# Kernel tuning notes

Hardware: AMD Instinct MI355X
Metric: run time of the kernel (lower is better)

The kernel has to match this reference:

```python
import jax, jax.numpy as jnp
import numpy as np

D_MODEL = 128
NHEAD = 8
HEAD_DIM = D_MODEL // NHEAD  # 16
NUM_LAYERS = 7
NUM_LABELS = 2
N_NODES = 10000
N_EDGES = 160000
NEG_SLOPE = 0.2  # GATv2Conv default negative_slope


def setup_inputs() -> dict:
    key = jax.random.key(0)
    ks = jax.random.split(key, 10)
    s = 1.0 / np.sqrt(D_MODEL)
    inp = {}
    inp["x"] = jax.random.normal(ks[0], (N_NODES, D_MODEL), dtype=jnp.float32)
    inp["edge_index"] = jax.random.randint(ks[1], (2, N_EDGES), 0, N_NODES, dtype=jnp.int64)
    inp["nchunks"] = 8  # uniform extra chunk size -> chunk = NUM_LABELS + 8 = 10
    # per-layer GATv2 params, stacked on a leading layer axis
    inp["Wl"] = jax.random.normal(ks[2], (NUM_LAYERS, D_MODEL, NHEAD * HEAD_DIM), dtype=jnp.float32) * s
    inp["bl"] = jnp.zeros((NUM_LAYERS, NHEAD * HEAD_DIM), dtype=jnp.float32)
    inp["Wr"] = jax.random.normal(ks[3], (NUM_LAYERS, D_MODEL, NHEAD * HEAD_DIM), dtype=jnp.float32) * s
    inp["br"] = jnp.zeros((NUM_LAYERS, NHEAD * HEAD_DIM), dtype=jnp.float32)
    inp["att"] = jax.random.normal(ks[4], (NUM_LAYERS, NHEAD, HEAD_DIM), dtype=jnp.float32) * s
    inp["bias"] = jnp.zeros((NUM_LAYERS, NHEAD * HEAD_DIM), dtype=jnp.float32)
    # split head: Linear(d_model, 1)
    inp["w_head"] = jax.random.normal(ks[5], (D_MODEL, 1), dtype=jnp.float32) * s
    inp["b_head"] = jnp.zeros((1,), dtype=jnp.float32)
    return inp


def _gatv2_layer(x, src, dst, Wl, bl, Wr, br, att, bias):
    # GATv2: e_ij = a^T LeakyReLU(W_l x_j + W_r x_i); alpha = segment-softmax over dst; out_i = sum alpha * W_l x_j
    N = x.shape[0]
    xl = (x @ Wl + bl).reshape(N, NHEAD, HEAD_DIM)
    xr = (x @ Wr + br).reshape(N, NHEAD, HEAD_DIM)
    z = jax.nn.leaky_relu(xl[src] + xr[dst], NEG_SLOPE)          # [E, H, D]
    e = jnp.einsum('ehd,hd->eh', z, att)                          # [E, H]
    emax = jax.ops.segment_max(e, dst, num_segments=N)            # [N, H]
    ex = jnp.exp(e - emax[dst])
    denom = jax.ops.segment_sum(ex, dst, num_segments=N)          # [N, H]
    alpha = ex / (denom[dst] + 1e-16)                             # [E, H]
    out = jax.ops.segment_sum(alpha[..., None] * xl[src], dst, num_segments=N)  # [N, H, D]
    return out.reshape(N, NHEAD * HEAD_DIM) + bias


def reference(x, edge_index, nchunks, Wl, bl, Wr, br, att, bias, w_head, b_head):
    N = x.shape[0]
    loop = jnp.arange(N, dtype=edge_index.dtype)  # GATv2Conv add_self_loops=True
    src = jnp.concatenate([edge_index[0], loop])
    dst = jnp.concatenate([edge_index[1], loop])
    for i in range(NUM_LAYERS):
        x = _gatv2_layer(x, src, dst, Wl[i], bl[i], Wr[i], br[i], att[i], bias[i])
    # uniform split of size (NUM_LABELS + nchunks); keep first NUM_LABELS rows of each chunk
    chunk = NUM_LABELS + int(nchunks)
    xs = x.reshape(-1, chunk, D_MODEL)[:, :NUM_LABELS]            # [n_chunks, num_labels, d]
    out = (xs @ w_head + b_head)[..., 0]                          # [n_chunks, num_labels]
    return out
```

## Files before the change

### kernel.cpp

```cpp
#include <hip/hip_runtime.h>
#include <math.h>

#define NT 256

typedef __attribute__((ext_vector_type(8))) short bf16x8;
typedef __attribute__((ext_vector_type(4))) float f32x4;


__device__ inline int detect_is64(const int* __restrict__ ei) {
    int is64 = 1;
#pragma unroll
    for (int k = 1; k < 16; k += 2) is64 &= (ei[k] == 0);
    return is64;
}

__device__ inline void split1(float f, short& hi, short& lo) {
    unsigned u = __float_as_uint(f);
    hi = (short)(u >> 16);
    float fl = f - __uint_as_float(u & 0xffff0000u);
    lo = (short)(__float_as_uint(fl) >> 16);
}

__device__ inline void cvt8(const float4& a, const float4& b, bf16x8& hi, bf16x8& lo) {
    float f[8] = {a.x, a.y, a.z, a.w, b.x, b.y, b.z, b.w};
#pragma unroll
    for (int j = 0; j < 8; j++) {
        unsigned u = __float_as_uint(f[j]);
        hi[j] = (short)(u >> 16);
        float fl = f[j] - __uint_as_float(u & 0xffff0000u);
        lo[j] = (short)(__float_as_uint(fl) >> 16);
    }
}


__global__ __launch_bounds__(256) void count_prep(const int* __restrict__ ei, int E, int N,
                                                  int* __restrict__ deg,
                                                  const float* __restrict__ Wl,
                                                  const float* __restrict__ Wr,
                                                  short* __restrict__ Whi,
                                                  short* __restrict__ Wlo) {
    __shared__ float Wt[128][17];
    int t = threadIdx.x;
    if (blockIdx.x < 112) {
        int l = blockIdx.x >> 4;
        int tile = blockIdx.x & 15;
        int c0 = tile * 16;
        const float* Wsrc = (c0 < 128) ? Wl + (size_t)l * 16384 : Wr + (size_t)l * 16384;
        int cbase = (c0 < 128) ? c0 : c0 - 128;
#pragma unroll
        for (int it = 0; it < 8; it++) {
            int idx = it * 256 + t;
            int k = idx >> 4, c = idx & 15;
            Wt[k][c] = Wsrc[(size_t)k * 128 + cbase + c];
        }
        __syncthreads();
        int kt = t >> 6, lane = t & 63, q = (lane >> 4), cl = lane & 15;
        bf16x8 hi, lo;
#pragma unroll
        for (int j = 0; j < 8; j++) {
            short h, lw;
            split1(Wt[kt * 32 + q * 8 + j][cl], h, lw);
            hi[j] = h; lo[j] = lw;
        }
        size_t off = ((((size_t)l * 16 + tile) * 4 + kt) * 64 + lane) * 8;
        *(bf16x8*)(Whi + off) = hi;
        *(bf16x8*)(Wlo + off) = lo;
    } else {
        int e = (blockIdx.x - 112) * 256 + t;
        if (e >= E) return;
        int is64 = detect_is64(ei);
        long long pos = (long long)E + e;
        int d = ei[is64 ? 2 * pos : pos];
        if ((unsigned)d < (unsigned)N) atomicAdd(&deg[d], 1);
    }
}

__global__ __launch_bounds__(256) void scan_kernel(const int* __restrict__ deg,
                                                   int* __restrict__ off,
                                                   int* __restrict__ cur, int N) {
    __shared__ int wsum[4];
    int t = threadIdx.x;
    int per = (N + 255) >> 8;
    int b0 = t * per;
    int s = 0;
    for (int k = 0; k < per; k++) {
        int idx = b0 + k;
        if (idx < N) s += deg[idx];
    }
    int lane = t & 63, w = t >> 6;
    int v = s;
#pragma unroll
    for (int o = 1; o < 64; o <<= 1) {
        int u = __shfl_up(v, o, 64);
        if (lane >= o) v += u;
    }
    if (lane == 63) wsum[w] = v;
    __syncthreads();
    if (t == 0) {
        int r = 0;
#pragma unroll
        for (int j = 0; j < 4; j++) { int xx = wsum[j]; wsum[j] = r; r += xx; }
        off[N] = r;
    }
    __syncthreads();
    int run = v - s + wsum[w];
    for (int k = 0; k < per; k++) {
        int idx = b0 + k;
        if (idx < N) {
            off[idx] = run;
            cur[idx] = run;
            run += deg[idx];
        }
    }
}

__global__ void fill_kernel(const int* __restrict__ ei, int E, int N,
                            int* __restrict__ cur, int* __restrict__ esrc) {
    int e = blockIdx.x * blockDim.x + threadIdx.x;
    if (e >= E) return;
    int is64 = detect_is64(ei);
    long long spos = e, dpos = (long long)E + e;
    int s = ei[is64 ? 2 * spos : spos];
    int d = ei[is64 ? 2 * dpos : dpos];
    if ((unsigned)d >= (unsigned)N || (unsigned)s >= (unsigned)N) return;
    int p = atomicAdd(&cur[d], 1);
    esrc[p] = s;
}


__global__ __launch_bounds__(512)
__attribute__((amdgpu_waves_per_eu(2, 2)))
void gemm_xlxr(const float* __restrict__ x,
               const short* __restrict__ WhiL,
               const short* __restrict__ WloL,
               const float* __restrict__ blv,
               const float* __restrict__ brv,
               float* __restrict__ xl,
               float* __restrict__ xr,
               int N, int ntiles) {
    int t = threadIdx.x;
    int w = t >> 6, lane = t & 63, q = lane >> 4, cl = lane & 15;

    bf16x8 Bh[2][4], Bl[2][4];
    float biasv[2];
    float* outp[2];
    int colc[2];
#pragma unroll
    for (int nt = 0; nt < 2; nt++) {
        int tile = w * 2 + nt;
        int col = tile * 16 + cl;
        if (col < 128) { biasv[nt] = blv[col]; outp[nt] = xl; colc[nt] = col; }
        else           { biasv[nt] = brv[col - 128]; outp[nt] = xr; colc[nt] = col - 128; }
#pragma unroll
        for (int kt = 0; kt < 4; kt++) {
            size_t off = (((size_t)tile * 4 + kt) * 64 + lane) * 8;
            Bh[nt][kt] = *(const bf16x8*)(WhiL + off);
            Bl[nt][kt] = *(const bf16x8*)(WloL + off);
        }
    }

    int rt = blockIdx.x;
    if (rt >= ntiles) return;
    float4 cur[8], nxt[8];
    {
        int row = rt * 16 + cl;
        if (row >= N) row = N - 1;
        const float* ap = x + (size_t)row * 128 + q * 8;
#pragma unroll
        for (int kt = 0; kt < 4; kt++) {
            cur[2 * kt]     = *(const float4*)(ap + kt * 32);
            cur[2 * kt + 1] = *(const float4*)(ap + kt * 32 + 4);
        }
    }

    for (; rt < ntiles; rt += gridDim.x) {
        int rn = rt + gridDim.x;
        if (rn < ntiles) {
            int row = rn * 16 + cl;
            if (row >= N) row = N - 1;
            const float* ap = x + (size_t)row * 128 + q * 8;
#pragma unroll
            for (int kt = 0; kt < 4; kt++) {
                nxt[2 * kt]     = *(const float4*)(ap + kt * 32);
                nxt[2 * kt + 1] = *(const float4*)(ap + kt * 32 + 4);
            }
        }

        bf16x8 Ah[4], Al[4];
#pragma unroll
        for (int kt = 0; kt < 4; kt++) cvt8(cur[2 * kt], cur[2 * kt + 1], Ah[kt], Al[kt]);

        f32x4 acc0 = {0.f, 0.f, 0.f, 0.f}, acc1 = {0.f, 0.f, 0.f, 0.f};
#pragma unroll
        for (int kt = 0; kt < 4; kt++) {
            acc0 = __builtin_amdgcn_mfma_f32_16x16x32_bf16(Ah[kt], Bh[0][kt], acc0, 0, 0, 0);
            acc1 = __builtin_amdgcn_mfma_f32_16x16x32_bf16(Ah[kt], Bh[1][kt], acc1, 0, 0, 0);
            acc0 = __builtin_amdgcn_mfma_f32_16x16x32_bf16(Al[kt], Bh[0][kt], acc0, 0, 0, 0);
            acc1 = __builtin_amdgcn_mfma_f32_16x16x32_bf16(Al[kt], Bh[1][kt], acc1, 0, 0, 0);
            acc0 = __builtin_amdgcn_mfma_f32_16x16x32_bf16(Ah[kt], Bl[0][kt], acc0, 0, 0, 0);
            acc1 = __builtin_amdgcn_mfma_f32_16x16x32_bf16(Ah[kt], Bl[1][kt], acc1, 0, 0, 0);
        }

#pragma unroll
        for (int nt = 0; nt < 2; nt++) {
            f32x4 a = nt ? acc1 : acc0;
#pragma unroll
            for (int r = 0; r < 4; r++) {
                int row = rt * 16 + q * 4 + r;
                if (row < N) outp[nt][(size_t)row * 128 + colc[nt]] = a[r] + biasv[nt];
            }
        }
#pragma unroll
        for (int j = 0; j < 8; j++) cur[j] = nxt[j];
    }
}


__global__ __launch_bounds__(256) void gat_agg(const float4* __restrict__ xl4,
                                               const float4* __restrict__ xr4,
                                               const int* __restrict__ off,
                                               const int* __restrict__ esrc,
                                               const float4* __restrict__ att4,
                                               const float4* __restrict__ bias4,
                                               float4* __restrict__ out4, int N) {
    int lane = threadIdx.x & 63;
    int sub = lane >> 4;
    int cl = lane & 15;
    int i = blockIdx.x * 4 + (threadIdx.x >> 6);
    if (i >= N) return;

    float4 xrA = xr4[(size_t)i * 32 + 2 * cl];
    float4 xrB = xr4[(size_t)i * 32 + 2 * cl + 1];
    float4 atA = att4[2 * cl];
    float4 atB = att4[2 * cl + 1];
    int start = off[i];
    int total = off[i + 1] - start + 1;
    int groups = (total + 3) >> 2;

    int k0 = sub;
    int s0 = (k0 < total) ? ((k0 == 0) ? i : esrc[start + k0 - 1]) : i;
    int k1 = 4 + sub;
    int s1 = (k1 < total) ? esrc[start + k1 - 1] : i;
    float4 v0A = xl4[(size_t)s0 * 32 + 2 * cl];
    float4 v0B = xl4[(size_t)s0 * 32 + 2 * cl + 1];
    int k2 = 8 + sub;
    int s2 = (k2 < total) ? esrc[start + k2 - 1] : i;
    float4 v1A = xl4[(size_t)s1 * 32 + 2 * cl];
    float4 v1B = xl4[(size_t)s1 * 32 + 2 * cl + 1];

    float s = 0.f;
    float4 aA = make_float4(0.f, 0.f, 0.f, 0.f);
    float4 aB = make_float4(0.f, 0.f, 0.f, 0.f);

    for (int g = 0; g < groups; g++) {
        int k3 = 4 * (g + 3) + sub;
        int s3 = (k3 < total) ? esrc[start + k3 - 1] : i;
        float4 v2A = xl4[(size_t)s2 * 32 + 2 * cl];
        float4 v2B = xl4[(size_t)s2 * 32 + 2 * cl + 1];

        int kc = 4 * g + sub;
        int valid = kc < total;
        float z0 = v0A.x + xrA.x, z1 = v0A.y + xrA.y, z2 = v0A.z + xrA.z, z3 = v0A.w + xrA.w;
        float z4 = v0B.x + xrB.x, z5 = v0B.y + xrB.y, z6 = v0B.z + xrB.z, z7 = v0B.w + xrB.w;
        z0 = (z0 > 0.f) ? z0 : 0.2f * z0;
        z1 = (z1 > 0.f) ? z1 : 0.2f * z1;
        z2 = (z2 > 0.f) ? z2 : 0.2f * z2;
        z3 = (z3 > 0.f) ? z3 : 0.2f * z3;
        z4 = (z4 > 0.f) ? z4 : 0.2f * z4;
        z5 = (z5 > 0.f) ? z5 : 0.2f * z5;
        z6 = (z6 > 0.f) ? z6 : 0.2f * z6;
        z7 = (z7 > 0.f) ? z7 : 0.2f * z7;
        float p = z0 * atA.x + z1 * atA.y + z2 * atA.z + z3 * atA.w
                + z4 * atB.x + z5 * atB.y + z6 * atB.z + z7 * atB.w;
        p += __shfl_xor(p, 1, 64);
        p = fminf(fmaxf(p, -80.f), 80.f);
        float wgt = valid ? __expf(p) : 0.f;
        s += wgt;
        aA.x += wgt * v0A.x; aA.y += wgt * v0A.y; aA.z += wgt * v0A.z; aA.w += wgt * v0A.w;
        aB.x += wgt * v0B.x; aB.y += wgt * v0B.y; aB.z += wgt * v0B.z; aB.w += wgt * v0B.w;

        v0A = v1A; v0B = v1B;
        v1A = v2A; v1B = v2B;
        s2 = s3;
    }

#pragma unroll
    for (int o = 16; o <= 32; o <<= 1) {
        s += __shfl_xor(s, o, 64);
        aA.x += __shfl_xor(aA.x, o, 64); aA.y += __shfl_xor(aA.y, o, 64);
        aA.z += __shfl_xor(aA.z, o, 64); aA.w += __shfl_xor(aA.w, o, 64);
        aB.x += __shfl_xor(aB.x, o, 64); aB.y += __shfl_xor(aB.y, o, 64);
        aB.z += __shfl_xor(aB.z, o, 64); aB.w += __shfl_xor(aB.w, o, 64);
    }
    if (sub == 0) {
        float inv = 1.f / (s + 1e-16f);
        float4 bA = bias4[2 * cl], bB = bias4[2 * cl + 1];
        float4 oA, oB;
        oA.x = aA.x * inv + bA.x; oA.y = aA.y * inv + bA.y;
        oA.z = aA.z * inv + bA.z; oA.w = aA.w * inv + bA.w;
        oB.x = aB.x * inv + bB.x; oB.y = aB.y * inv + bB.y;
        oB.z = aB.z * inv + bB.z; oB.w = aB.w * inv + bB.w;
        out4[(size_t)i * 32 + 2 * cl] = oA;
        out4[(size_t)i * 32 + 2 * cl + 1] = oB;
    }
}


__global__ __launch_bounds__(128) void head_kernel(const float* __restrict__ x,
                                                   const float* __restrict__ w,
                                                   const float* __restrict__ bh,
                                                   const int* __restrict__ nch,
                                                   float* __restrict__ out) {
    __shared__ float r[2];
    int b = blockIdx.x, t = threadIdx.x;
    int chunk = 2 + nch[0];
    int row = (b >> 1) * chunk + (b & 1);
    float p = x[(size_t)row * 128 + t] * w[t];
#pragma unroll
    for (int o = 32; o >= 1; o >>= 1) p += __shfl_xor(p, o, 64);
    if ((t & 63) == 0) r[t >> 6] = p;
    __syncthreads();
    if (t == 0) out[b] = r[0] + r[1] + bh[0];
}


extern "C" void kernel_launch(void* const* d_in, const int* in_sizes, int n_in,
                              void* d_out, int out_size, void* d_ws, size_t ws_size,
                              hipStream_t stream) {
    const float* x0 = (const float*)d_in[0];
    const int* ei = (const int*)d_in[1];
    const int* nchunks = (const int*)d_in[2];
    const float* Wl = (const float*)d_in[3];
    const float* bl = (const float*)d_in[4];
    const float* Wr = (const float*)d_in[5];
    const float* br = (const float*)d_in[6];
    const float* att = (const float*)d_in[7];
    const float* bias = (const float*)d_in[8];
    const float* wh = (const float*)d_in[9];
    const float* bh = (const float*)d_in[10];

    const int D = 128;
    int N = in_sizes[0] / D;
    int E = in_sizes[1] / 2;
    int ntiles = (N + 15) / 16;

    size_t fN = (size_t)N * D;
    const size_t WFRAG = 16 * 4 * 64 * 8;
    float* xl = (float*)d_ws;
    float* xr = xl + fN;
    float* xA = xr + fN;
    float* xB = xA + fN;
    short* Whi = (short*)(xB + fN);
    short* Wlo = Whi + 7 * WFRAG;
    int* deg = (int*)(Wlo + 7 * WFRAG);
    int* off = deg + N;
    int* cur = off + N + 1;
    int* esrc = cur + N;

    hipMemsetAsync(deg, 0, (size_t)N * sizeof(int), stream);
    count_prep<<<112 + (E + NT - 1) / NT, NT, 0, stream>>>(ei, E, N, deg, Wl, Wr, Whi, Wlo);
    scan_kernel<<<1, 256, 0, stream>>>(deg, off, cur, N);
    fill_kernel<<<(E + NT - 1) / NT, NT, 0, stream>>>(ei, E, N, cur, esrc);

    int aggblocks = (N + 3) / 4;
    const float* xc = x0;
    float* xn = xA;
    for (int l = 0; l < 7; l++) {
        gemm_xlxr<<<256, 512, 0, stream>>>(xc, Whi + (size_t)l * WFRAG, Wlo + (size_t)l * WFRAG,
                                           bl + (size_t)l * D, br + (size_t)l * D,
                                           xl, xr, N, ntiles);
        gat_agg<<<aggblocks, 256, 0, stream>>>((const float4*)xl, (const float4*)xr, off, esrc,
                                               (const float4*)(att + (size_t)l * D),
                                               (const float4*)(bias + (size_t)l * D),
                                               (float4*)xn, N);
        xc = xn;
        xn = (xn == xA) ? xB : xA;
    }
    head_kernel<<<out_size, 128, 0, stream>>>(xc, wh, bh, nchunks, (float*)d_out);
}
```

Before: 319.3 us.

## Remap gat_agg lanes to 8 edges per wave and fuse head into last layer

Changes the aggregation kernel so each wave handles 8 edges at once, with 8 lanes per edge and each lane covering one full head of 16 floats. This removes the cross-lane shuffle in the attention dot product but drops the software prefetch pipeline of neighbour rows. The final linear head is fused into the last layer's aggregation, which removes a separate kernel launch. The gemm launch attributes are also changed from waves_per_eu(2,2) to launch_bounds(512,1). The gather now loads 64 bytes per lane and needs more accumulator registers, which may lower occupancy.

```diff
diff --git a/kernel.cpp b/kernel.cpp
--- a/kernel.cpp
+++ b/kernel.cpp
@@ -128,19 +128,16 @@
 }
 
 
-__global__ __launch_bounds__(512)
-__attribute__((amdgpu_waves_per_eu(2, 2)))
-void gemm_xlxr(const float* __restrict__ x,
-               const short* __restrict__ WhiL,
-               const short* __restrict__ WloL,
-               const float* __restrict__ blv,
-               const float* __restrict__ brv,
-               float* __restrict__ xl,
-               float* __restrict__ xr,
-               int N, int ntiles) {
+__global__ __launch_bounds__(512, 1) void gemm_xlxr(const float* __restrict__ x,
+                                                    const short* __restrict__ WhiL,
+                                                    const short* __restrict__ WloL,
+                                                    const float* __restrict__ blv,
+                                                    const float* __restrict__ brv,
+                                                    float* __restrict__ xl,
+                                                    float* __restrict__ xr,
+                                                    int N, int ntiles) {
     int t = threadIdx.x;
     int w = t >> 6, lane = t & 63, q = lane >> 4, cl = lane & 15;
-
     bf16x8 Bh[2][4], Bl[2][4];
     float biasv[2];
     float* outp[2];
@@ -158,7 +155,6 @@
             Bl[nt][kt] = *(const bf16x8*)(WloL + off);
         }
     }
-
     int rt = blockIdx.x;
     if (rt >= ntiles) return;
     float4 cur[8], nxt[8];
@@ -172,7 +168,6 @@
             cur[2 * kt + 1] = *(const float4*)(ap + kt * 32 + 4);
         }
     }
-
     for (; rt < ntiles; rt += gridDim.x) {
         int rn = rt + gridDim.x;
         if (rn < ntiles) {
@@ -185,11 +180,9 @@
                 nxt[2 * kt + 1] = *(const float4*)(ap + kt * 32 + 4);
             }
         }
-
         bf16x8 Ah[4], Al[4];
 #pragma unroll
         for (int kt = 0; kt < 4; kt++) cvt8(cur[2 * kt], cur[2 * kt + 1], Ah[kt], Al[kt]);
-
         f32x4 acc0 = {0.f, 0.f, 0.f, 0.f}, acc1 = {0.f, 0.f, 0.f, 0.f};
 #pragma unroll
         for (int kt = 0; kt < 4; kt++) {
@@ -200,7 +193,6 @@
             acc0 = __builtin_amdgcn_mfma_f32_16x16x32_bf16(Ah[kt], Bl[0][kt], acc0, 0, 0, 0);
             acc1 = __builtin_amdgcn_mfma_f32_16x16x32_bf16(Ah[kt], Bl[1][kt], acc1, 0, 0, 0);
         }
-
 #pragma unroll
         for (int nt = 0; nt < 2; nt++) {
             f32x4 a = nt ? acc1 : acc0;
@@ -222,105 +214,103 @@
                                                const int* __restrict__ esrc,
                                                const float4* __restrict__ att4,
                                                const float4* __restrict__ bias4,
-                                               float4* __restrict__ out4, int N) {
+                                               float4* __restrict__ out4, int N,
+                                               int do_head,
+                                               const float* __restrict__ wh,
+                                               const float* __restrict__ bh,
+                                               const int* __restrict__ nch,
+                                               float* __restrict__ head_out) {
     int lane = threadIdx.x & 63;
-    int sub = lane >> 4;
-    int cl = lane & 15;
+    int sub = lane >> 3;
+    int hd = lane & 7;
     int i = blockIdx.x * 4 + (threadIdx.x >> 6);
     if (i >= N) return;
 
-    float4 xrA = xr4[(size_t)i * 32 + 2 * cl];
-    float4 xrB = xr4[(size_t)i * 32 + 2 * cl + 1];
-    float4 atA = att4[2 * cl];
-    float4 atB = att4[2 * cl + 1];
+    int base = hd * 4;
+    float4 xr0 = xr4[(size_t)i * 32 + base];
+    float4 xr1 = xr4[(size_t)i * 32 + base + 1];
+    float4 xr2 = xr4[(size_t)i * 32 + base + 2];
+    float4 xr3 = xr4[(size_t)i * 32 + base + 3];
+    float4 at0 = att4[base], at1 = att4[base + 1], at2 = att4[base + 2], at3 = att4[base + 3];
+
     int start = off[i];
     int total = off[i + 1] - start + 1;
-    int groups = (total + 3) >> 2;
-
-    int k0 = sub;
-    int s0 = (k0 < total) ? ((k0 == 0) ? i : esrc[start + k0 - 1]) : i;
-    int k1 = 4 + sub;
-    int s1 = (k1 < total) ? esrc[start + k1 - 1] : i;
-    float4 v0A = xl4[(size_t)s0 * 32 + 2 * cl];
-    float4 v0B = xl4[(size_t)s0 * 32 + 2 * cl + 1];
-    int k2 = 8 + sub;
-    int s2 = (k2 < total) ? esrc[start + k2 - 1] : i;
-    float4 v1A = xl4[(size_t)s1 * 32 + 2 * cl];
-    float4 v1B = xl4[(size_t)s1 * 32 + 2 * cl + 1];
+    int groups = (total + 7) >> 3;
 
     float s = 0.f;
-    float4 aA = make_float4(0.f, 0.f, 0.f, 0.f);
-    float4 aB = make_float4(0.f, 0.f, 0.f, 0.f);
+    float4 a0 = make_float4(0.f, 0.f, 0.f, 0.f);
+    float4 a1 = a0, a2 = a0, a3 = a0;
 
     for (int g = 0; g < groups; g++) {
-        int k3 = 4 * (g + 3) + sub;
-        int s3 = (k3 < total) ? esrc[start + k3 - 1] : i;
-        float4 v2A = xl4[(size_t)s2 * 32 + 2 * cl];
-        float4 v2B = xl4[(size_t)s2 * 32 + 2 * cl + 1];
-
-        int kc = 4 * g + sub;
-        int valid = kc < total;
-        float z0 = v0A.x + xrA.x, z1 = v0A.y + xrA.y, z2 = v0A.z + xrA.z, z3 = v0A.w + xrA.w;
-        float z4 = v0B.x + xrB.x, z5 = v0B.y + xrB.y, z6 = v0B.z + xrB.z, z7 = v0B.w + xrB.w;
-        z0 = (z0 > 0.f) ? z0 : 0.2f * z0;
-        z1 = (z1 > 0.f) ? z1 : 0.2f * z1;
-        z2 = (z2 > 0.f) ? z2 : 0.2f * z2;
-        z3 = (z3 > 0.f) ? z3 : 0.2f * z3;
-        z4 = (z4 > 0.f) ? z4 : 0.2f * z4;
-        z5 = (z5 > 0.f) ? z5 : 0.2f * z5;
-        z6 = (z6 > 0.f) ? z6 : 0.2f * z6;
-        z7 = (z7 > 0.f) ? z7 : 0.2f * z7;
-        float p = z0 * atA.x + z1 * atA.y + z2 * atA.z + z3 * atA.w
-                + z4 * atB.x + z5 * atB.y + z6 * atB.z + z7 * atB.w;
-        p += __shfl_xor(p, 1, 64);
+        int k = 8 * g + sub;
+        int valid = k < total;
+        int src = valid ? ((k == 0) ? i : esrc[start + k - 1]) : i;
+        const float4* vp = xl4 + (size_t)src * 32 + base;
+        float4 v0 = vp[0], v1 = vp[1], v2 = vp[2], v3 = vp[3];
+
+        float p = 0.f;
+#define LR(zv, xrv, atv)                                            \
+        {                                                            \
+            float z;                                                 \
+            z = zv.x + xrv.x; z = (z > 0.f) ? z : 0.2f * z; p += z * atv.x; \
+            z = zv.y + xrv.y; z = (z > 0.f) ? z : 0.2f * z; p += z * atv.y; \
+            z = zv.z + xrv.z; z = (z > 0.f) ? z : 0.2f * z; p += z * atv.z; \
+            z = zv.w + xrv.w; z = (z > 0.f) ? z : 0.2f * z; p += z * atv.w; \
+        }
+        LR(v0, xr0, at0) LR(v1, xr1, at1) LR(v2, xr2, at2) LR(v3, xr3, at3)
+#undef LR
         p = fminf(fmaxf(p, -80.f), 80.f);
         float wgt = valid ? __expf(p) : 0.f;
         s += wgt;
-        aA.x += wgt * v0A.x; aA.y += wgt * v0A.y; aA.z += wgt * v0A.z; aA.w += wgt * v0A.w;
-        aB.x += wgt * v0B.x; aB.y += wgt * v0B.y; aB.z += wgt * v0B.z; aB.w += wgt * v0B.w;
-
-        v0A = v1A; v0B = v1B;
-        v1A = v2A; v1B = v2B;
-        s2 = s3;
-    }
-
-#pragma unroll
-    for (int o = 16; o <= 32; o <<= 1) {
+        a0.x += wgt * v0.x; a0.y += wgt * v0.y; a0.z += wgt * v0.z; a0.w += wgt * v0.w;
+        a1.x += wgt * v1.x; a1.y += wgt * v1.y; a1.z += wgt * v1.z; a1.w += wgt * v1.w;
+        a2.x += wgt * v2.x; a2.y += wgt * v2.y; a2.z += wgt * v2.z; a2.w += wgt * v2.w;
+        a3.x += wgt * v3.x; a3.y += wgt * v3.y; a3.z += wgt * v3.z; a3.w += wgt * v3.w;
+    }
+
+#pragma unroll
+    for (int o = 8; o <= 32; o <<= 1) {
         s += __shfl_xor(s, o, 64);
-        aA.x += __shfl_xor(aA.x, o, 64); aA.y += __shfl_xor(aA.y, o, 64);
-        aA.z += __shfl_xor(aA.z, o, 64); aA.w += __shfl_xor(aA.w, o, 64);
-        aB.x += __shfl_xor(aB.x, o, 64); aB.y += __shfl_xor(aB.y, o, 64);
-        aB.z += __shfl_xor(aB.z, o, 64); aB.w += __shfl_xor(aB.w, o, 64);
-    }
-    if (sub == 0) {
-        float inv = 1.f / (s + 1e-16f);
-        float4 bA = bias4[2 * cl], bB = bias4[2 * cl + 1];
-        float4 oA, oB;
-        oA.x = aA.x * inv + bA.x; oA.y = aA.y * inv + bA.y;
-        oA.z = aA.z * inv + bA.z; oA.w = aA.w * inv + bA.w;
-        oB.x = aB.x * inv + bB.x; oB.y = aB.y * inv + bB.y;
-        oB.z = aB.z * inv + bB.z; oB.w = aB.w * inv + bB.w;
-        out4[(size_t)i * 32 + 2 * cl] = oA;
-        out4[(size_t)i * 32 + 2 * cl + 1] = oB;
-    }
-}
-
-
-__global__ __launch_bounds__(128) void head_kernel(const float* __restrict__ x,
-                                                   const float* __restrict__ w,
-                                                   const float* __restrict__ bh,
-                                                   const int* __restrict__ nch,
-                                                   float* __restrict__ out) {
-    __shared__ float r[2];
-    int b = blockIdx.x, t = threadIdx.x;
-    int chunk = 2 + nch[0];
-    int row = (b >> 1) * chunk + (b & 1);
-    float p = x[(size_t)row * 128 + t] * w[t];
-#pragma unroll
-    for (int o = 32; o >= 1; o >>= 1) p += __shfl_xor(p, o, 64);
-    if ((t & 63) == 0) r[t >> 6] = p;
-    __syncthreads();
-    if (t == 0) out[b] = r[0] + r[1] + bh[0];
+        a0.x += __shfl_xor(a0.x, o, 64); a0.y += __shfl_xor(a0.y, o, 64);
+        a0.z += __shfl_xor(a0.z, o, 64); a0.w += __shfl_xor(a0.w, o, 64);
+        a1.x += __shfl_xor(a1.x, o, 64); a1.y += __shfl_xor(a1.y, o, 64);
+        a1.z += __shfl_xor(a1.z, o, 64); a1.w += __shfl_xor(a1.w, o, 64);
+        a2.x += __shfl_xor(a2.x, o, 64); a2.y += __shfl_xor(a2.y, o, 64);
+        a2.z += __shfl_xor(a2.z, o, 64); a2.w += __shfl_xor(a2.w, o, 64);
+        a3.x += __shfl_xor(a3.x, o, 64); a3.y += __shfl_xor(a3.y, o, 64);
+        a3.z += __shfl_xor(a3.z, o, 64); a3.w += __shfl_xor(a3.w, o, 64);
+    }
+
+    float inv = 1.f / (s + 1e-16f);
+    float4 b0 = bias4[base], b1 = bias4[base + 1], b2 = bias4[base + 2], b3 = bias4[base + 3];
+    float4 o0, o1, o2, o3;
+    o0.x = a0.x * inv + b0.x; o0.y = a0.y * inv + b0.y; o0.z = a0.z * inv + b0.z; o0.w = a0.w * inv + b0.w;
+    o1.x = a1.x * inv + b1.x; o1.y = a1.y * inv + b1.y; o1.z = a1.z * inv + b1.z; o1.w = a1.w * inv + b1.w;
+    o2.x = a2.x * inv + b2.x; o2.y = a2.y * inv + b2.y; o2.z = a2.z * inv + b2.z; o2.w = a2.w * inv + b2.w;
+    o3.x = a3.x * inv + b3.x; o3.y = a3.y * inv + b3.y; o3.z = a3.z * inv + b3.z; o3.w = a3.w * inv + b3.w;
+
+    if (!do_head) {
+        if (sub == 0) {
+            float4* op = out4 + (size_t)i * 32 + base;
+            op[0] = o0; op[1] = o1; op[2] = o2; op[3] = o3;
+        }
+    } else {
+        int chunk = 2 + nch[0];
+        int ci = i / chunk;
+        int m = i - ci * chunk;
+        if (m < 2) {
+            const float4* wv = (const float4*)wh + base;
+            float4 w0 = wv[0], w1 = wv[1], w2 = wv[2], w3 = wv[3];
+            float p = o0.x * w0.x + o0.y * w0.y + o0.z * w0.z + o0.w * w0.w
+                    + o1.x * w1.x + o1.y * w1.y + o1.z * w1.z + o1.w * w1.w
+                    + o2.x * w2.x + o2.y * w2.y + o2.z * w2.z + o2.w * w2.w
+                    + o3.x * w3.x + o3.y * w3.y + o3.z * w3.z + o3.w * w3.w;
+            p += __shfl_xor(p, 1, 64);
+            p += __shfl_xor(p, 2, 64);
+            p += __shfl_xor(p, 4, 64);
+            if (lane == 0) head_out[ci * 2 + m] = p + bh[0];
+        }
+    }
 }
 
 
@@ -366,15 +356,16 @@
     const float* xc = x0;
     float* xn = xA;
     for (int l = 0; l < 7; l++) {
+        int last = (l == 6);
         gemm_xlxr<<<256, 512, 0, stream>>>(xc, Whi + (size_t)l * WFRAG, Wlo + (size_t)l * WFRAG,
                                            bl + (size_t)l * D, br + (size_t)l * D,
                                            xl, xr, N, ntiles);
         gat_agg<<<aggblocks, 256, 0, stream>>>((const float4*)xl, (const float4*)xr, off, esrc,
                                                (const float4*)(att + (size_t)l * D),
                                                (const float4*)(bias + (size_t)l * D),
-                                               (float4*)xn, N);
+                                               (float4*)xn, N,
+                                               last, wh, bh, nchunks, (float*)d_out);
         xc = xn;
         xn = (xn == xA) ? xB : xA;
     }
-    head_kernel<<<out_size, 128, 0, stream>>>(xc, wh, bh, nchunks, (float*)d_out);
-}
+}
```

New measurement: 359.5 us. +12.6%, slower.

## Fuse CSR build into one cooperative kernel and fold head into last aggregation

Applied to the files above, without the earlier changes.

The memset, degree count, scan and fill launches are replaced by a single cooperative kernel that uses grid-wide syncs, with the old multi-launch path kept as a fallback. The split-head linear projection moves into the final gat_agg launch, which removes the separate head kernel. The gemm launch bounds change from waves_per_eu(2,2) to launch_bounds(512,1). The goal is to cut launch overhead and small-kernel gaps, at the cost of running the scan inside a single block while the rest of the grid waits at a grid sync.

```diff
diff --git a/kernel.cpp b/kernel.cpp
--- a/kernel.cpp
+++ b/kernel.cpp
@@ -1,5 +1,8 @@
 #include <hip/hip_runtime.h>
+#include <hip/hip_cooperative_groups.h>
 #include <math.h>
+
+namespace cg = cooperative_groups;
 
 #define NT 256
 
@@ -29,6 +32,109 @@
         hi[j] = (short)(u >> 16);
         float fl = f[j] - __uint_as_float(u & 0xffff0000u);
         lo[j] = (short)(__float_as_uint(fl) >> 16);
+    }
+}
+
+__device__ inline void prep_w_block(int bid, const float* __restrict__ Wl,
+                                    const float* __restrict__ Wr,
+                                    short* __restrict__ Whi, short* __restrict__ Wlo,
+                                    float (*Wt)[17], int t) {
+    int l = bid >> 4;
+    int tile = bid & 15;
+    int c0 = tile * 16;
+    const float* Wsrc = (c0 < 128) ? Wl + (size_t)l * 16384 : Wr + (size_t)l * 16384;
+    int cbase = (c0 < 128) ? c0 : c0 - 128;
+#pragma unroll
+    for (int it = 0; it < 8; it++) {
+        int idx = it * 256 + t;
+        int k = idx >> 4, c = idx & 15;
+        Wt[k][c] = Wsrc[(size_t)k * 128 + cbase + c];
+    }
+    __syncthreads();
+    int kt = t >> 6, lane = t & 63, q = (lane >> 4), cl = lane & 15;
+    bf16x8 hi, lo;
+#pragma unroll
+    for (int j = 0; j < 8; j++) {
+        short h, lw;
+        split1(Wt[kt * 32 + q * 8 + j][cl], h, lw);
+        hi[j] = h; lo[j] = lw;
+    }
+    size_t off = ((((size_t)l * 16 + tile) * 4 + kt) * 64 + lane) * 8;
+    *(bf16x8*)(Whi + off) = hi;
+    *(bf16x8*)(Wlo + off) = lo;
+}
+
+
+__global__ __launch_bounds__(256) void csr_build(const int* __restrict__ ei, int E, int N,
+                                                 int* __restrict__ deg, int* __restrict__ off,
+                                                 int* __restrict__ cur, int* __restrict__ esrc,
+                                                 const float* __restrict__ Wl,
+                                                 const float* __restrict__ Wr,
+                                                 short* __restrict__ Whi,
+                                                 short* __restrict__ Wlo) {
+    cg::grid_group grid = cg::this_grid();
+    __shared__ float Wt[128][17];
+    __shared__ int wsum[4];
+    int t = threadIdx.x;
+    int b = blockIdx.x;
+    int gt = b * 256 + t;
+    const int GT = gridDim.x * 256;
+    int is64 = detect_is64(ei);
+
+    for (int i = gt; i < N; i += GT) deg[i] = 0;
+    if (b < 112) prep_w_block(b, Wl, Wr, Whi, Wlo, Wt, t);
+    grid.sync();
+
+    for (int e = gt; e < E; e += GT) {
+        long long pos = (long long)E + e;
+        int d = ei[is64 ? 2 * pos : pos];
+        if ((unsigned)d < (unsigned)N) atomicAdd(&deg[d], 1);
+    }
+    grid.sync();
+
+    if (b == 0) {
+        int per = (N + 255) >> 8;
+        int b0 = t * per;
+        int s = 0;
+        for (int k = 0; k < per; k++) {
+            int idx = b0 + k;
+            if (idx < N) s += deg[idx];
+        }
+        int lane = t & 63, w = t >> 6;
+        int v = s;
+#pragma unroll
+        for (int o = 1; o < 64; o <<= 1) {
+            int u = __shfl_up(v, o, 64);
+            if (lane >= o) v += u;
+        }
+        if (lane == 63) wsum[w] = v;
+        __syncthreads();
+        if (t == 0) {
+            int r = 0;
+#pragma unroll
+            for (int j = 0; j < 4; j++) { int xx = wsum[j]; wsum[j] = r; r += xx; }
+            off[N] = r;
+        }
+        __syncthreads();
+        int run = v - s + wsum[w];
+        for (int k = 0; k < per; k++) {
+            int idx = b0 + k;
+            if (idx < N) {
+                off[idx] = run;
+                cur[idx] = run;
+                run += deg[idx];
+            }
+        }
+    }
+    grid.sync();
+
+    for (int e = gt; e < E; e += GT) {
+        long long spos = e, dpos = (long long)E + e;
+        int s = ei[is64 ? 2 * spos : spos];
+        int d = ei[is64 ? 2 * dpos : dpos];
+        if ((unsigned)d >= (unsigned)N || (unsigned)s >= (unsigned)N) continue;
+        int p = atomicAdd(&cur[d], 1);
+        esrc[p] = s;
     }
 }
 
@@ -42,29 +148,7 @@
     __shared__ float Wt[128][17];
     int t = threadIdx.x;
     if (blockIdx.x < 112) {
-        int l = blockIdx.x >> 4;
-        int tile = blockIdx.x & 15;
-        int c0 = tile * 16;
-        const float* Wsrc = (c0 < 128) ? Wl + (size_t)l * 16384 : Wr + (size_t)l * 16384;
-        int cbase = (c0 < 128) ? c0 : c0 - 128;
-#pragma unroll
-        for (int it = 0; it < 8; it++) {
-            int idx = it * 256 + t;
-            int k = idx >> 4, c = idx & 15;
-            Wt[k][c] = Wsrc[(size_t)k * 128 + cbase + c];
-        }
-        __syncthreads();
-        int kt = t >> 6, lane = t & 63, q = (lane >> 4), cl = lane & 15;
-        bf16x8 hi, lo;
-#pragma unroll
-        for (int j = 0; j < 8; j++) {
-            short h, lw;
-            split1(Wt[kt * 32 + q * 8 + j][cl], h, lw);
-            hi[j] = h; lo[j] = lw;
-        }
-        size_t off = ((((size_t)l * 16 + tile) * 4 + kt) * 64 + lane) * 8;
-        *(bf16x8*)(Whi + off) = hi;
-        *(bf16x8*)(Wlo + off) = lo;
+        prep_w_block(blockIdx.x, Wl, Wr, Whi, Wlo, Wt, t);
     } else {
         int e = (blockIdx.x - 112) * 256 + t;
         if (e >= E) return;
@@ -128,19 +212,16 @@
 }
 
 
-__global__ __launch_bounds__(512)
-__attribute__((amdgpu_waves_per_eu(2, 2)))
-void gemm_xlxr(const float* __restrict__ x,
-               const short* __restrict__ WhiL,
-               const short* __restrict__ WloL,
-               const float* __restrict__ blv,
-               const float* __restrict__ brv,
-               float* __restrict__ xl,
-               float* __restrict__ xr,
-               int N, int ntiles) {
+__global__ __launch_bounds__(512, 1) void gemm_xlxr(const float* __restrict__ x,
+                                                    const short* __restrict__ WhiL,
+                                                    const short* __restrict__ WloL,
+                                                    const float* __restrict__ blv,
+                                                    const float* __restrict__ brv,
+                                                    float* __restrict__ xl,
+                                                    float* __restrict__ xr,
+                                                    int N, int ntiles) {
     int t = threadIdx.x;
     int w = t >> 6, lane = t & 63, q = lane >> 4, cl = lane & 15;
-
     bf16x8 Bh[2][4], Bl[2][4];
     float biasv[2];
     float* outp[2];
@@ -158,7 +239,6 @@
             Bl[nt][kt] = *(const bf16x8*)(WloL + off);
         }
     }
-
     int rt = blockIdx.x;
     if (rt >= ntiles) return;
     float4 cur[8], nxt[8];
@@ -172,7 +252,6 @@
             cur[2 * kt + 1] = *(const float4*)(ap + kt * 32 + 4);
         }
     }
-
     for (; rt < ntiles; rt += gridDim.x) {
         int rn = rt + gridDim.x;
         if (rn < ntiles) {
@@ -185,11 +264,9 @@
                 nxt[2 * kt + 1] = *(const float4*)(ap + kt * 32 + 4);
             }
         }
-
         bf16x8 Ah[4], Al[4];
 #pragma unroll
         for (int kt = 0; kt < 4; kt++) cvt8(cur[2 * kt], cur[2 * kt + 1], Ah[kt], Al[kt]);
-
         f32x4 acc0 = {0.f, 0.f, 0.f, 0.f}, acc1 = {0.f, 0.f, 0.f, 0.f};
 #pragma unroll
         for (int kt = 0; kt < 4; kt++) {
@@ -200,7 +277,6 @@
             acc0 = __builtin_amdgcn_mfma_f32_16x16x32_bf16(Ah[kt], Bl[0][kt], acc0, 0, 0, 0);
             acc1 = __builtin_amdgcn_mfma_f32_16x16x32_bf16(Ah[kt], Bl[1][kt], acc1, 0, 0, 0);
         }
-
 #pragma unroll
         for (int nt = 0; nt < 2; nt++) {
             f32x4 a = nt ? acc1 : acc0;
@@ -222,7 +298,12 @@
                                                const int* __restrict__ esrc,
                                                const float4* __restrict__ att4,
                                                const float4* __restrict__ bias4,
-                                               float4* __restrict__ out4, int N) {
+                                               float4* __restrict__ out4, int N,
+                                               int do_head,
+                                               const float* __restrict__ wh,
+                                               const float* __restrict__ bh,
+                                               const int* __restrict__ nch,
+                                               float* __restrict__ head_out) {
     int lane = threadIdx.x & 63;
     int sub = lane >> 4;
     int cl = lane & 15;
@@ -292,35 +373,36 @@
         aB.x += __shfl_xor(aB.x, o, 64); aB.y += __shfl_xor(aB.y, o, 64);
         aB.z += __shfl_xor(aB.z, o, 64); aB.w += __shfl_xor(aB.w, o, 64);
     }
-    if (sub == 0) {
-        float inv = 1.f / (s + 1e-16f);
-        float4 bA = bias4[2 * cl], bB = bias4[2 * cl + 1];
-        float4 oA, oB;
-        oA.x = aA.x * inv + bA.x; oA.y = aA.y * inv + bA.y;
-        oA.z = aA.z * inv + bA.z; oA.w = aA.w * inv + bA.w;
-        oB.x = aB.x * inv + bB.x; oB.y = aB.y * inv + bB.y;
-        oB.z = aB.z * inv + bB.z; oB.w = aB.w * inv + bB.w;
-        out4[(size_t)i * 32 + 2 * cl] = oA;
-        out4[(size_t)i * 32 + 2 * cl + 1] = oB;
-    }
-}
-
-
-__global__ __launch_bounds__(128) void head_kernel(const float* __restrict__ x,
-                                                   const float* __restrict__ w,
-                                                   const float* __restrict__ bh,
-                                                   const int* __restrict__ nch,
-                                                   float* __restrict__ out) {
-    __shared__ float r[2];
-    int b = blockIdx.x, t = threadIdx.x;
-    int chunk = 2 + nch[0];
-    int row = (b >> 1) * chunk + (b & 1);
-    float p = x[(size_t)row * 128 + t] * w[t];
-#pragma unroll
-    for (int o = 32; o >= 1; o >>= 1) p += __shfl_xor(p, o, 64);
-    if ((t & 63) == 0) r[t >> 6] = p;
-    __syncthreads();
-    if (t == 0) out[b] = r[0] + r[1] + bh[0];
+
+    float inv = 1.f / (s + 1e-16f);
+    float4 bA = bias4[2 * cl], bB = bias4[2 * cl + 1];
+    float4 oA, oB;
+    oA.x = aA.x * inv + bA.x; oA.y = aA.y * inv + bA.y;
+    oA.z = aA.z * inv + bA.z; oA.w = aA.w * inv + bA.w;
+    oB.x = aB.x * inv + bB.x; oB.y = aB.y * inv + bB.y;
+    oB.z = aB.z * inv + bB.z; oB.w = aB.w * inv + bB.w;
+
+    if (!do_head) {
+        if (sub == 0) {
+            out4[(size_t)i * 32 + 2 * cl] = oA;
+            out4[(size_t)i * 32 + 2 * cl + 1] = oB;
+        }
+    } else {
+        int chunk = 2 + nch[0];
+        int ci = i / chunk;
+        int m = i - ci * chunk;
+        if (m < 2) {
+            const float4* wv = (const float4*)wh;
+            float4 wA = wv[2 * cl], wB = wv[2 * cl + 1];
+            float p = oA.x * wA.x + oA.y * wA.y + oA.z * wA.z + oA.w * wA.w
+                    + oB.x * wB.x + oB.y * wB.y + oB.z * wB.z + oB.w * wB.w;
+            p += __shfl_xor(p, 1, 64);
+            p += __shfl_xor(p, 2, 64);
+            p += __shfl_xor(p, 4, 64);
+            p += __shfl_xor(p, 8, 64);
+            if (lane == 0) head_out[ci * 2 + m] = p + bh[0];
+        }
+    }
 }
 
 
@@ -357,24 +439,34 @@
     int* cur = off + N + 1;
     int* esrc = cur + N;
 
-    hipMemsetAsync(deg, 0, (size_t)N * sizeof(int), stream);
-    count_prep<<<112 + (E + NT - 1) / NT, NT, 0, stream>>>(ei, E, N, deg, Wl, Wr, Whi, Wlo);
-    scan_kernel<<<1, 256, 0, stream>>>(deg, off, cur, N);
-    fill_kernel<<<(E + NT - 1) / NT, NT, 0, stream>>>(ei, E, N, cur, esrc);
+    void* args[] = {
+        (void*)&ei, (void*)&E, (void*)&N,
+        (void*)&deg, (void*)&off, (void*)&cur, (void*)&esrc,
+        (void*)&Wl, (void*)&Wr, (void*)&Whi, (void*)&Wlo
+    };
+    hipError_t rc = hipLaunchCooperativeKernel((void*)csr_build, dim3(256), dim3(256),
+                                               args, 0, stream);
+    if (rc != hipSuccess) {
+        hipMemsetAsync(deg, 0, (size_t)N * sizeof(int), stream);
+        count_prep<<<112 + (E + NT - 1) / NT, NT, 0, stream>>>(ei, E, N, deg, Wl, Wr, Whi, Wlo);
+        scan_kernel<<<1, 256, 0, stream>>>(deg, off, cur, N);
+        fill_kernel<<<(E + NT - 1) / NT, NT, 0, stream>>>(ei, E, N, cur, esrc);
+    }
 
     int aggblocks = (N + 3) / 4;
     const float* xc = x0;
     float* xn = xA;
     for (int l = 0; l < 7; l++) {
+        int last = (l == 6);
         gemm_xlxr<<<256, 512, 0, stream>>>(xc, Whi + (size_t)l * WFRAG, Wlo + (size_t)l * WFRAG,
                                            bl + (size_t)l * D, br + (size_t)l * D,
                                            xl, xr, N, ntiles);
         gat_agg<<<aggblocks, 256, 0, stream>>>((const float4*)xl, (const float4*)xr, off, esrc,
                                                (const float4*)(att + (size_t)l * D),
                                                (const float4*)(bias + (size_t)l * D),
-                                               (float4*)xn, N);
+                                               (float4*)xn, N,
+                                               last, wh, bh, nchunks, (float*)d_out);
         xc = xn;
         xn = (xn == xA) ? xB : xA;
     }
-    head_kernel<<<out_size, 128, 0, stream>>>(xc, wh, bh, nchunks, (float*)d_out);
-}
+}
```

Measured after the change: 415.0 us. 1.3x slower.
